# Kernel optimization log

Measured on AMD Instinct MI355X. Metric: run time of the kernel, lower is better.

The kernel has to match this reference:

```python
import jax, jax.numpy as jnp
import numpy as np

C_Z = 128
N_HEADS = 4
HEAD_DIM = 32
TOTAL = N_HEADS * HEAD_DIM
B, N = 1, 256


def setup_inputs() -> dict:
    key = jax.random.key(0)
    ks = jax.random.split(key, 10)
    s = lambda k, sh: jax.random.normal(k, sh, dtype=jnp.float32) * 0.02
    return {
        "pair_representation": jax.random.normal(ks[0], (B, N, N, C_Z), dtype=jnp.float32),
        "ln_gamma": jnp.ones((C_Z,), jnp.float32),
        "ln_beta": jnp.zeros((C_Z,), jnp.float32),
        "Wq": s(ks[1], (C_Z, TOTAL)),
        "Wk": s(ks[2], (C_Z, TOTAL)),
        "Wv": s(ks[3], (C_Z, TOTAL)),
        "Wb": s(ks[4], (C_Z, N_HEADS)),
        "Wg": s(ks[5], (C_Z, TOTAL)),
        "bg": jnp.zeros((TOTAL,), jnp.float32),
        "Wo": s(ks[6], (TOTAL, C_Z)),
        "bo": jnp.zeros((C_Z,), jnp.float32),
    }


def reference(pair_representation, ln_gamma, ln_beta, Wq, Wk, Wv, Wb, Wg, bg, Wo, bo):
    x = pair_representation
    # LayerNorm over c_z
    mu = jnp.mean(x, axis=-1, keepdims=True)
    var = jnp.mean((x - mu) ** 2, axis=-1, keepdims=True)
    x = (x - mu) * jax.lax.rsqrt(var + 1e-5) * ln_gamma + ln_beta

    b, n, _, _ = x.shape
    split = lambda t: t.reshape(b, n, n, N_HEADS, HEAD_DIM)
    Q = split(x @ Wq)  # [b,i,j,h,d]
    K = split(x @ Wk)
    V = split(x @ Wv)
    G = jax.nn.sigmoid(split(x @ Wg + bg))
    Bias = x @ Wb  # [b,j,k,h]

    scores = jnp.einsum("bijhd,bikhd->bijkh", Q, K) / np.float32(np.sqrt(HEAD_DIM))
    scores = scores + Bias[:, None]  # broadcast over i
    attn = jax.nn.softmax(scores, axis=3)  # over k
    vals = jnp.einsum("bijkh,bikhd->bijhd", attn, V)
    vals = (G * vals).reshape(b, n, n, TOTAL)
    return vals @ Wo + bo
```

## Files before the change

kernel.cpp:

```cpp
#include <hip/hip_runtime.h>
#include <hip/hip_bf16.h>


#define QSCALE 0.17677669529663687f

typedef __attribute__((ext_vector_type(8))) short bf16x8;
typedef __attribute__((ext_vector_type(4))) float f32x4;

__device__ __forceinline__ ushort f2bf(float f) {
    uint32_t u = __builtin_bit_cast(uint32_t, f);
    uint32_t r = (u + 0x7FFFu + ((u >> 16) & 1u)) >> 16;
    return (ushort)r;
}
__device__ __forceinline__ float bf2f(ushort b) {
    return __builtin_bit_cast(float, ((uint32_t)b) << 16);
}
__device__ __forceinline__ uint pk2(float a, float b) {
    union { __hip_bfloat162 h; uint u; } cv;
    cv.h = __float22bfloat162_rn(make_float2(a, b));
    return cv.u;
}
__device__ __forceinline__ float4 ld4f(const float* p) { return *(const float4*)p; }

__global__ __launch_bounds__(256) void prep_kernel(
    const float* __restrict__ Wq, const float* __restrict__ Wk, const float* __restrict__ Wv,
    const float* __restrict__ Wb, const float* __restrict__ Wg, const float* __restrict__ Wo,
    ushort* __restrict__ Wfrag, ushort* __restrict__ WoFrag)
{
    int idx = blockIdx.x * 256 + threadIdx.x;
    if (idx < 67584) {
        int j = idx & 7, lane = (idx >> 3) & 63, ks = (idx >> 9) & 3, ct = idx >> 11;
        int n = ct * 16 + (lane & 15);
        int k = ks * 32 + (lane >> 4) * 8 + j;
        float v = 0.f;
        if (n < 128)      v = Wq[k * 128 + n] * QSCALE;
        else if (n < 256) v = Wk[k * 128 + (n - 128)];
        else if (n < 384) v = Wv[k * 128 + (n - 256)];
        else if (n < 512) v = Wg[k * 128 + (n - 384)];
        else if (n < 516) v = Wb[k * 4 + (n - 512)];
        Wfrag[idx] = f2bf(v);
    } else {
        int idx2 = idx - 67584;
        int j = idx2 & 7, lane = (idx2 >> 3) & 63, ks = (idx2 >> 9) & 3, ct = idx2 >> 11;
        int n = ct * 16 + (lane & 15);
        int k = ks * 32 + (lane >> 4) * 8 + j;
        WoFrag[idx2] = f2bf(Wo[k * 128 + n]);
    }
}

__global__ __launch_bounds__(256) void proj_kernel(
    const float* __restrict__ x, const float* __restrict__ gamma, const float* __restrict__ beta,
    const ushort* __restrict__ Wfrag, const float* __restrict__ bg,
    ushort* __restrict__ Qg, ushort* __restrict__ Kg, ushort* __restrict__ Vtg,
    ushort* __restrict__ Gg, float* __restrict__ BbF)
{
    __shared__ ushort Bs[11 * 2048];
    const int t = threadIdx.x;
    const int wave = t >> 6, lane = t & 63, m = lane & 15, quad = lane >> 4;
    const int p0 = blockIdx.x * 64;
    const int arow = p0 + wave * 16 + m;

    float4 xa[4][2];
    float sum = 0.f, ssq = 0.f;
#pragma unroll
    for (int ks = 0; ks < 4; ++ks) {
        const float* rp = x + arow * 128 + ks * 32 + quad * 8;
        xa[ks][0] = ld4f(rp);
        xa[ks][1] = ld4f(rp + 4);
#pragma unroll
        for (int q4 = 0; q4 < 2; ++q4) {
            float4 v = xa[ks][q4];
            sum += v.x + v.y + v.z + v.w;
            ssq += v.x * v.x + v.y * v.y + v.z * v.z + v.w * v.w;
        }
    }
    sum += __shfl_xor(sum, 16); ssq += __shfl_xor(ssq, 16);
    sum += __shfl_xor(sum, 32); ssq += __shfl_xor(ssq, 32);
    const float mu   = sum * (1.f / 128.f);
    const float var  = ssq * (1.f / 128.f) - mu * mu;
    const float rstd = rsqrtf(var + 1e-5f);

    bf16x8 xf[4];
#pragma unroll
    for (int ks = 0; ks < 4; ++ks) {
        union { bf16x8 v; uint u[4]; } xu;
#pragma unroll
        for (int q4 = 0; q4 < 2; ++q4) {
            const int c = ks * 32 + quad * 8 + q4 * 4;
            float4 g4 = ld4f(gamma + c);
            float4 b4 = ld4f(beta + c);
            float4 v = xa[ks][q4];
            float n0 = (v.x - mu) * rstd * g4.x + b4.x;
            float n1 = (v.y - mu) * rstd * g4.y + b4.y;
            float n2 = (v.z - mu) * rstd * g4.z + b4.z;
            float n3 = (v.w - mu) * rstd * g4.w + b4.w;
            xu.u[q4 * 2]     = pk2(n0, n1);
            xu.u[q4 * 2 + 1] = pk2(n2, n3);
        }
        xf[ks] = xu.v;
    }

    const int p = arow;
    const int i = p >> 8, j2 = p & 255;

    for (int phase = 0; phase < 3; ++phase) {
        const int ctbase = phase * 11;
        __syncthreads();
        const uint4* src = (const uint4*)(Wfrag + ctbase * 2048);
        uint4* dst = (uint4*)Bs;
#pragma unroll
        for (int r = 0; r < 11; ++r) dst[r * 256 + t] = src[r * 256 + t];
        __syncthreads();

        for (int ctl = 0; ctl < 11; ++ctl) {
            const int ct = ctbase + ctl;
            f32x4 acc = (f32x4){0.f, 0.f, 0.f, 0.f};
#pragma unroll
            for (int ks = 0; ks < 4; ++ks) {
                bf16x8 wfr = ((const bf16x8*)Bs)[(ctl * 4 + ks) * 64 + lane];
                acc = __builtin_amdgcn_mfma_f32_16x16x32_bf16(wfr, xf[ks], acc, 0, 0, 0);
            }
            if (ct < 32) {
                const int cls = ct >> 3;
                const int npb = (ct & 7) * 16 + quad * 4;
                const int hh = npb >> 5, d0 = npb & 31;
                if (cls == 2) {
                    const int vb = ((i * 4 + hh) * 32 + d0) * 256 + j2;
#pragma unroll
                    for (int r = 0; r < 4; ++r)
                        Vtg[vb + r * 256] = f2bf(acc[r]);
                } else {
                    const int off = ((i * 4 + hh) * 256 + j2) * 32 + d0;
                    uint2 u;
                    if (cls == 3) {
                        float4 bg4 = ld4f(&bg[npb]);
                        float z0 = 1.f / (1.f + __expf(-(acc[0] + bg4.x)));
                        float z1 = 1.f / (1.f + __expf(-(acc[1] + bg4.y)));
                        float z2 = 1.f / (1.f + __expf(-(acc[2] + bg4.z)));
                        float z3 = 1.f / (1.f + __expf(-(acc[3] + bg4.w)));
                        u.x = pk2(z0, z1); u.y = pk2(z2, z3);
                        *(uint2*)(&Gg[off]) = u;
                    } else {
                        u.x = pk2(acc[0], acc[1]); u.y = pk2(acc[2], acc[3]);
                        if (cls == 0) *(uint2*)(&Qg[off]) = u;
                        else          *(uint2*)(&Kg[off]) = u;
                    }
                }
            } else if (quad == 0) {
#pragma unroll
                for (int r = 0; r < 4; ++r) {
                    int addr = (((r * 16 + (i >> 4)) * 16 + (j2 >> 4)) * 64 +
                                ((j2 & 15) >> 2) * 16 + (i & 15)) * 4 + (j2 & 3);
                    BbF[addr] = acc[r];
                }
            }
        }
    }
}

__global__ __launch_bounds__(256) void attn_kernel(
    const ushort* __restrict__ Qg, const ushort* __restrict__ Kg, const ushort* __restrict__ Vtg,
    const ushort* __restrict__ Gg, const float* __restrict__ BbF, ushort* __restrict__ gvals)
{
    __shared__ ushort Pl[4][64 * 72];
    const int t = threadIdx.x;
    const int wave = t >> 6, lane = t & 63, m = lane & 15, quad = lane >> 4;
    const int ih = blockIdx.x, i = ih >> 2, h = ih & 3;

    const int j0 = wave * 64;
    bf16x8 qf[4];
#pragma unroll
    for (int jt = 0; jt < 4; ++jt)
        qf[jt] = *(const bf16x8*)(Qg + ih * 8192 + (j0 + jt * 16 + m) * 32 + quad * 8);

    f32x4 O[4][2];
    float lsum[4];
#pragma unroll
    for (int jt = 0; jt < 4; ++jt) {
        O[jt][0] = (f32x4){0.f, 0.f, 0.f, 0.f};
        O[jt][1] = (f32x4){0.f, 0.f, 0.f, 0.f};
        lsum[jt] = 0.f;
    }

    for (int kt2 = 0; kt2 < 4; ++kt2) {
        const int k0 = kt2 * 64;
        bf16x8 kf[4];
#pragma unroll
        for (int kk = 0; kk < 4; ++kk)
            kf[kk] = *(const bf16x8*)(Kg + ih * 8192 + (k0 + kk * 16 + m) * 32 + quad * 8);

#pragma unroll
        for (int jt = 0; jt < 4; ++jt) {
            const int jtg = wave * 4 + jt;
#pragma unroll
            for (int kk = 0; kk < 4; ++kk) {
                const int ktg = kt2 * 4 + kk;
                f32x4 bias = *(const f32x4*)(BbF + (((h * 16 + jtg) * 16 + ktg) * 64 + lane) * 4);
                f32x4 S = __builtin_amdgcn_mfma_f32_16x16x32_bf16(kf[kk], qf[jt], bias, 0, 0, 0);
                float pv0 = __expf(S[0]);
                float pv1 = __expf(S[1]);
                float pv2 = __expf(S[2]);
                float pv3 = __expf(S[3]);
                lsum[jt] += pv0 + pv1 + pv2 + pv3;
                uint2 u; u.x = pk2(pv0, pv1); u.y = pk2(pv2, pv3);
                *(uint2*)(&Pl[wave][(jt * 16 + m) * 72 + kk * 16 + quad * 4]) = u;
            }
        }
#pragma unroll
        for (int kc = 0; kc < 2; ++kc) {
            bf16x8 pf[4], vf[2];
#pragma unroll
            for (int jt = 0; jt < 4; ++jt)
                pf[jt] = *(const bf16x8*)(&Pl[wave][(jt * 16 + m) * 72 + kc * 32 + quad * 8]);
#pragma unroll
            for (int dt = 0; dt < 2; ++dt)
                vf[dt] = *(const bf16x8*)(Vtg + (ih * 32 + dt * 16 + m) * 256 + k0 + kc * 32 + quad * 8);
#pragma unroll
            for (int jt = 0; jt < 4; ++jt)
#pragma unroll
                for (int dt = 0; dt < 2; ++dt)
                    O[jt][dt] = __builtin_amdgcn_mfma_f32_16x16x32_bf16(
                        vf[dt], pf[jt], O[jt][dt], 0, 0, 0);
        }
    }

#pragma unroll
    for (int jt = 0; jt < 4; ++jt) {
        float s = lsum[jt];
        s += __shfl_xor(s, 16);
        s += __shfl_xor(s, 32);
        lsum[jt] = 1.f / s;
    }

#pragma unroll
    for (int jt = 0; jt < 4; ++jt) {
        const int j = j0 + jt * 16 + m;
        const float rl = lsum[jt];
#pragma unroll
        for (int dt = 0; dt < 2; ++dt) {
            const int d0 = dt * 16 + quad * 4;
            ushort4 gv = *(const ushort4*)(&Gg[ih * 8192 + j * 32 + d0]);
            float v0 = O[jt][dt][0] * rl * bf2f(gv.x);
            float v1 = O[jt][dt][1] * rl * bf2f(gv.y);
            float v2 = O[jt][dt][2] * rl * bf2f(gv.z);
            float v3 = O[jt][dt][3] * rl * bf2f(gv.w);
            uint2 u; u.x = pk2(v0, v1); u.y = pk2(v2, v3);
            *(uint2*)(&gvals[(i * 256 + j) * 128 + h * 32 + d0]) = u;
        }
    }
}

__global__ __launch_bounds__(256) void oproj_kernel(
    const ushort* __restrict__ gvals, const ushort* __restrict__ WoFrag,
    const float* __restrict__ bo, float* __restrict__ out)
{
    __shared__ ushort Bs[8 * 2048];
    const int t = threadIdx.x;
    const int wave = t >> 6, lane = t & 63, m = lane & 15, quad = lane >> 4;
    const int p0 = blockIdx.x * 64;
    {
        const uint4* src = (const uint4*)WoFrag;
        uint4* dst = (uint4*)Bs;
#pragma unroll
        for (int r = 0; r < 8; ++r) dst[r * 256 + t] = src[r * 256 + t];
    }
    bf16x8 gf[4];
    const int p = p0 + wave * 16 + m;
#pragma unroll
    for (int ks = 0; ks < 4; ++ks)
        gf[ks] = *(const bf16x8*)(gvals + p * 128 + ks * 32 + quad * 8);
    __syncthreads();

#pragma unroll
    for (int ct = 0; ct < 8; ++ct) {
        f32x4 acc = (f32x4){0.f, 0.f, 0.f, 0.f};
#pragma unroll
        for (int ks = 0; ks < 4; ++ks) {
            bf16x8 wfr = ((const bf16x8*)Bs)[(ct * 4 + ks) * 64 + lane];
            acc = __builtin_amdgcn_mfma_f32_16x16x32_bf16(wfr, gf[ks], acc, 0, 0, 0);
        }
        const int c0 = ct * 16 + quad * 4;
        float4 bov = ld4f(&bo[c0]);
        float4 v = make_float4(acc[0] + bov.x, acc[1] + bov.y,
                               acc[2] + bov.z, acc[3] + bov.w);
        *(float4*)(&out[p * 128 + c0]) = v;
    }
}

extern "C" void kernel_launch(void* const* d_in, const int* in_sizes, int n_in,
                              void* d_out, int out_size, void* d_ws, size_t ws_size,
                              hipStream_t stream) {
    const float* x     = (const float*)d_in[0];
    const float* gamma = (const float*)d_in[1];
    const float* beta  = (const float*)d_in[2];
    const float* Wq    = (const float*)d_in[3];
    const float* Wk    = (const float*)d_in[4];
    const float* Wv    = (const float*)d_in[5];
    const float* Wb    = (const float*)d_in[6];
    const float* Wg    = (const float*)d_in[7];
    const float* bg    = (const float*)d_in[8];
    const float* Wo    = (const float*)d_in[9];
    const float* bo    = (const float*)d_in[10];

    ushort* ws     = (ushort*)d_ws;
    ushort* Wfrag  = ws;
    ushort* WoFrag = Wfrag + 67584;
    ushort* Qg     = WoFrag + 16384;
    ushort* Kg     = Qg + 8388608;
    ushort* Vtg    = Kg + 8388608;
    ushort* Gg     = Vtg + 8388608;
    ushort* gvals  = Gg + 8388608;
    float*  BbF    = (float*)(gvals + 8388608);

    prep_kernel<<<328, 256, 0, stream>>>(Wq, Wk, Wv, Wb, Wg, Wo, Wfrag, WoFrag);
    proj_kernel<<<1024, 256, 0, stream>>>(x, gamma, beta, Wfrag, bg, Qg, Kg, Vtg, Gg, BbF);
    attn_kernel<<<1024, 256, 0, stream>>>(Qg, Kg, Vtg, Gg, BbF, gvals);
    oproj_kernel<<<1024, 256, 0, stream>>>(gvals, WoFrag, bo, (float*)d_out);
}
```

Before: 171.2 us.

## Fuse projection, attention and output projection into one per-row kernel

Replaces the separate projection, attention and output-projection kernels with a single kernel per row i using 1024 threads. It computes K, V, Q and G for each head on the fly into shared memory and registers, runs softmax attention, then applies the output projection from shared memory. The pair bias moves to a small standalone kernel. This removes the large global round-trips of Q/K/V/G/gvals, in exchange for only 256 blocks, heavy register use, and weights read straight from global memory rather than staged in LDS.

```diff
diff --git a/kernel.cpp b/kernel.cpp
--- a/kernel.cpp
+++ b/kernel.cpp
@@ -12,9 +12,6 @@
     uint32_t r = (u + 0x7FFFu + ((u >> 16) & 1u)) >> 16;
     return (ushort)r;
 }
-__device__ __forceinline__ float bf2f(ushort b) {
-    return __builtin_bit_cast(float, ((uint32_t)b) << 16);
-}
 __device__ __forceinline__ uint pk2(float a, float b) {
     union { __hip_bfloat162 h; uint u; } cv;
     cv.h = __float22bfloat162_rn(make_float2(a, b));
@@ -22,253 +19,262 @@
 }
 __device__ __forceinline__ float4 ld4f(const float* p) { return *(const float4*)p; }
 
+__device__ __forceinline__ bf16x8 xpose(uint2 A, uint2 B, int quad, int m) {
+    int s0 = ((quad & 1) << 5) + m;
+    int s1 = s0 + 16;
+    uint a0 = (uint)__shfl((int)A.x, s0), a1 = (uint)__shfl((int)A.y, s0);
+    uint a2 = (uint)__shfl((int)A.x, s1), a3 = (uint)__shfl((int)A.y, s1);
+    uint b0 = (uint)__shfl((int)B.x, s0), b1 = (uint)__shfl((int)B.y, s0);
+    uint b2 = (uint)__shfl((int)B.x, s1), b3 = (uint)__shfl((int)B.y, s1);
+    bool lo = quad < 2;
+    union { bf16x8 v; uint u[4]; } r;
+    r.u[0] = lo ? a0 : b0;
+    r.u[1] = lo ? a1 : b1;
+    r.u[2] = lo ? a2 : b2;
+    r.u[3] = lo ? a3 : b3;
+    return r.v;
+}
+
 __global__ __launch_bounds__(256) void prep_kernel(
     const float* __restrict__ Wq, const float* __restrict__ Wk, const float* __restrict__ Wv,
-    const float* __restrict__ Wb, const float* __restrict__ Wg, const float* __restrict__ Wo,
+    const float* __restrict__ Wg, const float* __restrict__ Wo,
     ushort* __restrict__ Wfrag, ushort* __restrict__ WoFrag)
 {
     int idx = blockIdx.x * 256 + threadIdx.x;
-    if (idx < 67584) {
-        int j = idx & 7, lane = (idx >> 3) & 63, ks = (idx >> 9) & 3, ct = idx >> 11;
+    if (idx < 65536) {
+        int e = idx & 7, lane = (idx >> 3) & 63, ks = (idx >> 9) & 3, ct = idx >> 11;
         int n = ct * 16 + (lane & 15);
-        int k = ks * 32 + (lane >> 4) * 8 + j;
-        float v = 0.f;
+        int k = ks * 32 + (lane >> 4) * 8 + e;
+        float v;
         if (n < 128)      v = Wq[k * 128 + n] * QSCALE;
         else if (n < 256) v = Wk[k * 128 + (n - 128)];
         else if (n < 384) v = Wv[k * 128 + (n - 256)];
-        else if (n < 512) v = Wg[k * 128 + (n - 384)];
-        else if (n < 516) v = Wb[k * 4 + (n - 512)];
+        else              v = Wg[k * 128 + (n - 384)];
         Wfrag[idx] = f2bf(v);
     } else {
-        int idx2 = idx - 67584;
-        int j = idx2 & 7, lane = (idx2 >> 3) & 63, ks = (idx2 >> 9) & 3, ct = idx2 >> 11;
+        int idx2 = idx - 65536;
+        int e = idx2 & 7, lane = (idx2 >> 3) & 63, ks = (idx2 >> 9) & 3, ct = idx2 >> 11;
         int n = ct * 16 + (lane & 15);
-        int k = ks * 32 + (lane >> 4) * 8 + j;
+        int k = ks * 32 + (lane >> 4) * 8 + e;
         WoFrag[idx2] = f2bf(Wo[k * 128 + n]);
     }
 }
 
-__global__ __launch_bounds__(256) void proj_kernel(
-    const float* __restrict__ x, const float* __restrict__ gamma, const float* __restrict__ beta,
-    const ushort* __restrict__ Wfrag, const float* __restrict__ bg,
-    ushort* __restrict__ Qg, ushort* __restrict__ Kg, ushort* __restrict__ Vtg,
-    ushort* __restrict__ Gg, float* __restrict__ BbF)
+__global__ __launch_bounds__(256) void bias_kernel(
+    const float* __restrict__ x, const float* __restrict__ gamma,
+    const float* __restrict__ beta, const float* __restrict__ Wb,
+    float* __restrict__ BbF)
 {
-    __shared__ ushort Bs[11 * 2048];
     const int t = threadIdx.x;
-    const int wave = t >> 6, lane = t & 63, m = lane & 15, quad = lane >> 4;
-    const int p0 = blockIdx.x * 64;
-    const int arow = p0 + wave * 16 + m;
-
+    const int p = blockIdx.x * 128 + (t >> 1);
+    const int half = t & 1;
+    const float* rp = x + p * 128 + half * 64;
+    float4 v[16];
+    float sum = 0.f, ssq = 0.f;
+#pragma unroll
+    for (int ii = 0; ii < 16; ++ii) {
+        v[ii] = ld4f(rp + ii * 4);
+        sum += v[ii].x + v[ii].y + v[ii].z + v[ii].w;
+        ssq += v[ii].x * v[ii].x + v[ii].y * v[ii].y + v[ii].z * v[ii].z + v[ii].w * v[ii].w;
+    }
+    sum += __shfl_xor(sum, 1);
+    ssq += __shfl_xor(ssq, 1);
+    float mu = sum * (1.f / 128.f);
+    float var = ssq * (1.f / 128.f) - mu * mu;
+    float rstd = rsqrtf(var + 1e-5f);
+
+    float d0 = 0.f, d1 = 0.f, d2 = 0.f, d3 = 0.f;
+#pragma unroll
+    for (int ii = 0; ii < 16; ++ii) {
+        int c = half * 64 + ii * 4;
+        float4 g4 = ld4f(gamma + c), b4 = ld4f(beta + c);
+        float n0 = (v[ii].x - mu) * rstd * g4.x + b4.x;
+        float n1 = (v[ii].y - mu) * rstd * g4.y + b4.y;
+        float n2 = (v[ii].z - mu) * rstd * g4.z + b4.z;
+        float n3 = (v[ii].w - mu) * rstd * g4.w + b4.w;
+        float4 w0 = ld4f(Wb + (c + 0) * 4);
+        float4 w1 = ld4f(Wb + (c + 1) * 4);
+        float4 w2 = ld4f(Wb + (c + 2) * 4);
+        float4 w3 = ld4f(Wb + (c + 3) * 4);
+        d0 += n0 * w0.x + n1 * w1.x + n2 * w2.x + n3 * w3.x;
+        d1 += n0 * w0.y + n1 * w1.y + n2 * w2.y + n3 * w3.y;
+        d2 += n0 * w0.z + n1 * w1.z + n2 * w2.z + n3 * w3.z;
+        d3 += n0 * w0.w + n1 * w1.w + n2 * w2.w + n3 * w3.w;
+    }
+    d0 += __shfl_xor(d0, 1);
+    d1 += __shfl_xor(d1, 1);
+    d2 += __shfl_xor(d2, 1);
+    d3 += __shfl_xor(d3, 1);
+    if (half == 0) {
+        int j = p >> 8, k = p & 255;
+        int base = ((j >> 4) * 16 + (k >> 4)) * 256 + ((k & 15) >> 2) * 64 + (j & 15) * 4 + (k & 3);
+        BbF[base]          = d0;
+        BbF[base + 65536]  = d1;
+        BbF[base + 131072] = d2;
+        BbF[base + 196608] = d3;
+    }
+}
+
+__global__ __launch_bounds__(1024) void fused_kernel(
+    const float* __restrict__ x, const float* __restrict__ gamma,
+    const float* __restrict__ beta, const ushort* __restrict__ Wfrag,
+    const float* __restrict__ bg, const float* __restrict__ BbF,
+    const ushort* __restrict__ WoFrag, const float* __restrict__ bo,
+    float* __restrict__ out)
+{
+    __shared__ ushort smem[32768];
+    ushort* K_s = smem;
+    ushort* V_s = smem + 8192;
+    ushort* GV_s = smem;
+
+    const int t = threadIdx.x;
+    const int w = t >> 6, lane = t & 63, m = lane & 15, quad = lane >> 4;
+    const int i = blockIdx.x;
+
+    const float* xr = x + (i * 256 + w * 16 + m) * 128 + quad * 8;
     float4 xa[4][2];
     float sum = 0.f, ssq = 0.f;
 #pragma unroll
     for (int ks = 0; ks < 4; ++ks) {
-        const float* rp = x + arow * 128 + ks * 32 + quad * 8;
-        xa[ks][0] = ld4f(rp);
-        xa[ks][1] = ld4f(rp + 4);
+        xa[ks][0] = ld4f(xr + ks * 32);
+        xa[ks][1] = ld4f(xr + ks * 32 + 4);
 #pragma unroll
         for (int q4 = 0; q4 < 2; ++q4) {
-            float4 v = xa[ks][q4];
-            sum += v.x + v.y + v.z + v.w;
-            ssq += v.x * v.x + v.y * v.y + v.z * v.z + v.w * v.w;
+            float4 vv = xa[ks][q4];
+            sum += vv.x + vv.y + vv.z + vv.w;
+            ssq += vv.x * vv.x + vv.y * vv.y + vv.z * vv.z + vv.w * vv.w;
         }
     }
     sum += __shfl_xor(sum, 16); ssq += __shfl_xor(ssq, 16);
     sum += __shfl_xor(sum, 32); ssq += __shfl_xor(ssq, 32);
-    const float mu   = sum * (1.f / 128.f);
-    const float var  = ssq * (1.f / 128.f) - mu * mu;
+    const float mu = sum * (1.f / 128.f);
+    const float var = ssq * (1.f / 128.f) - mu * mu;
     const float rstd = rsqrtf(var + 1e-5f);
 
-    bf16x8 xf[4];
+    bf16x8 xnf[4];
 #pragma unroll
     for (int ks = 0; ks < 4; ++ks) {
+        const int c = ks * 32 + quad * 8;
+        float4 g0 = ld4f(gamma + c), g1 = ld4f(gamma + c + 4);
+        float4 b0 = ld4f(beta + c),  b1 = ld4f(beta + c + 4);
+        float4 v0 = xa[ks][0], v1 = xa[ks][1];
         union { bf16x8 v; uint u[4]; } xu;
-#pragma unroll
-        for (int q4 = 0; q4 < 2; ++q4) {
-            const int c = ks * 32 + quad * 8 + q4 * 4;
-            float4 g4 = ld4f(gamma + c);
-            float4 b4 = ld4f(beta + c);
-            float4 v = xa[ks][q4];
-            float n0 = (v.x - mu) * rstd * g4.x + b4.x;
-            float n1 = (v.y - mu) * rstd * g4.y + b4.y;
-            float n2 = (v.z - mu) * rstd * g4.z + b4.z;
-            float n3 = (v.w - mu) * rstd * g4.w + b4.w;
-            xu.u[q4 * 2]     = pk2(n0, n1);
-            xu.u[q4 * 2 + 1] = pk2(n2, n3);
-        }
-        xf[ks] = xu.v;
-    }
-
-    const int p = arow;
-    const int i = p >> 8, j2 = p & 255;
-
-    for (int phase = 0; phase < 3; ++phase) {
-        const int ctbase = phase * 11;
+        xu.u[0] = pk2((v0.x - mu) * rstd * g0.x + b0.x, (v0.y - mu) * rstd * g0.y + b0.y);
+        xu.u[1] = pk2((v0.z - mu) * rstd * g0.z + b0.z, (v0.w - mu) * rstd * g0.w + b0.w);
+        xu.u[2] = pk2((v1.x - mu) * rstd * g1.x + b1.x, (v1.y - mu) * rstd * g1.y + b1.y);
+        xu.u[3] = pk2((v1.z - mu) * rstd * g1.z + b1.z, (v1.w - mu) * rstd * g1.w + b1.w);
+        xnf[ks] = xu.v;
+    }
+
+    uint gst[4][4];
+
+#pragma unroll
+    for (int h = 0; h < 4; ++h) {
+#pragma unroll
+        for (int dt = 0; dt < 2; ++dt) {
+            const int ct = 8 + 2 * h + dt;
+            f32x4 acc = (f32x4){0.f, 0.f, 0.f, 0.f};
+#pragma unroll
+            for (int ks = 0; ks < 4; ++ks) {
+                bf16x8 wf = *(const bf16x8*)(Wfrag + ((ct * 4 + ks) * 64 + lane) * 8);
+                acc = __builtin_amdgcn_mfma_f32_16x16x32_bf16(wf, xnf[ks], acc, 0, 0, 0);
+            }
+            uint2 u; u.x = pk2(acc[0], acc[1]); u.y = pk2(acc[2], acc[3]);
+            *(uint2*)(K_s + (w * 64 + (dt * 2 + (quad >> 1)) * 16 + m) * 8 + (quad & 1) * 4) = u;
+        }
+#pragma unroll
+        for (int dt = 0; dt < 2; ++dt) {
+            const int ct = 16 + 2 * h + dt;
+            f32x4 acc = (f32x4){0.f, 0.f, 0.f, 0.f};
+#pragma unroll
+            for (int ks = 0; ks < 4; ++ks) {
+                bf16x8 wf = *(const bf16x8*)(Wfrag + ((ct * 4 + ks) * 64 + lane) * 8);
+                acc = __builtin_amdgcn_mfma_f32_16x16x32_bf16(xnf[ks], wf, acc, 0, 0, 0);
+            }
+            uint2 u; u.x = pk2(acc[0], acc[1]); u.y = pk2(acc[2], acc[3]);
+            *(uint2*)(V_s + (((w >> 1) * 2 + dt) * 512 +
+                             (((w & 1) * 2 + (quad >> 1)) * 16 + m) * 8 + (quad & 1) * 4)) = u;
+        }
+        uint2 qpk[2];
+#pragma unroll
+        for (int dt = 0; dt < 2; ++dt) {
+            const int ct = 2 * h + dt;
+            f32x4 acc = (f32x4){0.f, 0.f, 0.f, 0.f};
+#pragma unroll
+            for (int ks = 0; ks < 4; ++ks) {
+                bf16x8 wf = *(const bf16x8*)(Wfrag + ((ct * 4 + ks) * 64 + lane) * 8);
+                acc = __builtin_amdgcn_mfma_f32_16x16x32_bf16(wf, xnf[ks], acc, 0, 0, 0);
+            }
+            qpk[dt].x = pk2(acc[0], acc[1]); qpk[dt].y = pk2(acc[2], acc[3]);
+        }
+        bf16x8 qf = xpose(qpk[0], qpk[1], quad, m);
+        f32x4 Gs[2];
+#pragma unroll
+        for (int dt = 0; dt < 2; ++dt) {
+            const int ct = 24 + 2 * h + dt;
+            f32x4 acc = (f32x4){0.f, 0.f, 0.f, 0.f};
+#pragma unroll
+            for (int ks = 0; ks < 4; ++ks) {
+                bf16x8 wf = *(const bf16x8*)(Wfrag + ((ct * 4 + ks) * 64 + lane) * 8);
+                acc = __builtin_amdgcn_mfma_f32_16x16x32_bf16(wf, xnf[ks], acc, 0, 0, 0);
+            }
+            float4 bg4 = ld4f(bg + h * 32 + dt * 16 + quad * 4);
+            Gs[dt][0] = 1.f / (1.f + __expf(-(acc[0] + bg4.x)));
+            Gs[dt][1] = 1.f / (1.f + __expf(-(acc[1] + bg4.y)));
+            Gs[dt][2] = 1.f / (1.f + __expf(-(acc[2] + bg4.z)));
+            Gs[dt][3] = 1.f / (1.f + __expf(-(acc[3] + bg4.w)));
+        }
+
         __syncthreads();
-        const uint4* src = (const uint4*)(Wfrag + ctbase * 2048);
-        uint4* dst = (uint4*)Bs;
-#pragma unroll
-        for (int r = 0; r < 11; ++r) dst[r * 256 + t] = src[r * 256 + t];
+
+        f32x4 O0 = (f32x4){0.f, 0.f, 0.f, 0.f};
+        f32x4 O1 = (f32x4){0.f, 0.f, 0.f, 0.f};
+        float lsum = 0.f;
+        const float* bb = BbF + ((h * 16 + w) * 16) * 256 + lane * 4;
+#pragma unroll
+        for (int kt2 = 0; kt2 < 4; ++kt2) {
+            uint2 spk[4];
+#pragma unroll
+            for (int kk = 0; kk < 4; ++kk) {
+                const int tile = kt2 * 4 + kk;
+                bf16x8 kf = *(const bf16x8*)(K_s + (tile * 64 + lane) * 8);
+                f32x4 bias = *(const f32x4*)(bb + tile * 256);
+                f32x4 S = __builtin_amdgcn_mfma_f32_16x16x32_bf16(kf, qf, bias, 0, 0, 0);
+                float p0 = __expf(S[0]), p1 = __expf(S[1]);
+                float p2 = __expf(S[2]), p3 = __expf(S[3]);
+                lsum += p0 + p1 + p2 + p3;
+                spk[kk].x = pk2(p0, p1); spk[kk].y = pk2(p2, p3);
+            }
+#pragma unroll
+            for (int kc = 0; kc < 2; ++kc) {
+                bf16x8 pf = xpose(spk[kc * 2], spk[kc * 2 + 1], quad, m);
+                const int kcg = kt2 * 2 + kc;
+                bf16x8 vf0 = *(const bf16x8*)(V_s + ((kcg * 2 + 0) * 512 + lane * 8));
+                bf16x8 vf1 = *(const bf16x8*)(V_s + ((kcg * 2 + 1) * 512 + lane * 8));
+                O0 = __builtin_amdgcn_mfma_f32_16x16x32_bf16(vf0, pf, O0, 0, 0, 0);
+                O1 = __builtin_amdgcn_mfma_f32_16x16x32_bf16(vf1, pf, O1, 0, 0, 0);
+            }
+        }
+        lsum += __shfl_xor(lsum, 16);
+        lsum += __shfl_xor(lsum, 32);
+        const float rl = 1.f / lsum;
+        gst[h][0] = pk2(O0[0] * rl * Gs[0][0], O0[1] * rl * Gs[0][1]);
+        gst[h][1] = pk2(O0[2] * rl * Gs[0][2], O0[3] * rl * Gs[0][3]);
+        gst[h][2] = pk2(O1[0] * rl * Gs[1][0], O1[1] * rl * Gs[1][1]);
+        gst[h][3] = pk2(O1[2] * rl * Gs[1][2], O1[3] * rl * Gs[1][3]);
+
         __syncthreads();
-
-        for (int ctl = 0; ctl < 11; ++ctl) {
-            const int ct = ctbase + ctl;
-            f32x4 acc = (f32x4){0.f, 0.f, 0.f, 0.f};
-#pragma unroll
-            for (int ks = 0; ks < 4; ++ks) {
-                bf16x8 wfr = ((const bf16x8*)Bs)[(ctl * 4 + ks) * 64 + lane];
-                acc = __builtin_amdgcn_mfma_f32_16x16x32_bf16(wfr, xf[ks], acc, 0, 0, 0);
-            }
-            if (ct < 32) {
-                const int cls = ct >> 3;
-                const int npb = (ct & 7) * 16 + quad * 4;
-                const int hh = npb >> 5, d0 = npb & 31;
-                if (cls == 2) {
-                    const int vb = ((i * 4 + hh) * 32 + d0) * 256 + j2;
-#pragma unroll
-                    for (int r = 0; r < 4; ++r)
-                        Vtg[vb + r * 256] = f2bf(acc[r]);
-                } else {
-                    const int off = ((i * 4 + hh) * 256 + j2) * 32 + d0;
-                    uint2 u;
-                    if (cls == 3) {
-                        float4 bg4 = ld4f(&bg[npb]);
-                        float z0 = 1.f / (1.f + __expf(-(acc[0] + bg4.x)));
-                        float z1 = 1.f / (1.f + __expf(-(acc[1] + bg4.y)));
-                        float z2 = 1.f / (1.f + __expf(-(acc[2] + bg4.z)));
-                        float z3 = 1.f / (1.f + __expf(-(acc[3] + bg4.w)));
-                        u.x = pk2(z0, z1); u.y = pk2(z2, z3);
-                        *(uint2*)(&Gg[off]) = u;
-                    } else {
-                        u.x = pk2(acc[0], acc[1]); u.y = pk2(acc[2], acc[3]);
-                        if (cls == 0) *(uint2*)(&Qg[off]) = u;
-                        else          *(uint2*)(&Kg[off]) = u;
-                    }
-                }
-            } else if (quad == 0) {
-#pragma unroll
-                for (int r = 0; r < 4; ++r) {
-                    int addr = (((r * 16 + (i >> 4)) * 16 + (j2 >> 4)) * 64 +
-                                ((j2 & 15) >> 2) * 16 + (i & 15)) * 4 + (j2 & 3);
-                    BbF[addr] = acc[r];
-                }
-            }
-        }
-    }
-}
-
-__global__ __launch_bounds__(256) void attn_kernel(
-    const ushort* __restrict__ Qg, const ushort* __restrict__ Kg, const ushort* __restrict__ Vtg,
-    const ushort* __restrict__ Gg, const float* __restrict__ BbF, ushort* __restrict__ gvals)
-{
-    __shared__ ushort Pl[4][64 * 72];
-    const int t = threadIdx.x;
-    const int wave = t >> 6, lane = t & 63, m = lane & 15, quad = lane >> 4;
-    const int ih = blockIdx.x, i = ih >> 2, h = ih & 3;
-
-    const int j0 = wave * 64;
-    bf16x8 qf[4];
-#pragma unroll
-    for (int jt = 0; jt < 4; ++jt)
-        qf[jt] = *(const bf16x8*)(Qg + ih * 8192 + (j0 + jt * 16 + m) * 32 + quad * 8);
-
-    f32x4 O[4][2];
-    float lsum[4];
-#pragma unroll
-    for (int jt = 0; jt < 4; ++jt) {
-        O[jt][0] = (f32x4){0.f, 0.f, 0.f, 0.f};
-        O[jt][1] = (f32x4){0.f, 0.f, 0.f, 0.f};
-        lsum[jt] = 0.f;
-    }
-
-    for (int kt2 = 0; kt2 < 4; ++kt2) {
-        const int k0 = kt2 * 64;
-        bf16x8 kf[4];
-#pragma unroll
-        for (int kk = 0; kk < 4; ++kk)
-            kf[kk] = *(const bf16x8*)(Kg + ih * 8192 + (k0 + kk * 16 + m) * 32 + quad * 8);
-
-#pragma unroll
-        for (int jt = 0; jt < 4; ++jt) {
-            const int jtg = wave * 4 + jt;
-#pragma unroll
-            for (int kk = 0; kk < 4; ++kk) {
-                const int ktg = kt2 * 4 + kk;
-                f32x4 bias = *(const f32x4*)(BbF + (((h * 16 + jtg) * 16 + ktg) * 64 + lane) * 4);
-                f32x4 S = __builtin_amdgcn_mfma_f32_16x16x32_bf16(kf[kk], qf[jt], bias, 0, 0, 0);
-                float pv0 = __expf(S[0]);
-                float pv1 = __expf(S[1]);
-                float pv2 = __expf(S[2]);
-                float pv3 = __expf(S[3]);
-                lsum[jt] += pv0 + pv1 + pv2 + pv3;
-                uint2 u; u.x = pk2(pv0, pv1); u.y = pk2(pv2, pv3);
-                *(uint2*)(&Pl[wave][(jt * 16 + m) * 72 + kk * 16 + quad * 4]) = u;
-            }
-        }
-#pragma unroll
-        for (int kc = 0; kc < 2; ++kc) {
-            bf16x8 pf[4], vf[2];
-#pragma unroll
-            for (int jt = 0; jt < 4; ++jt)
-                pf[jt] = *(const bf16x8*)(&Pl[wave][(jt * 16 + m) * 72 + kc * 32 + quad * 8]);
-#pragma unroll
-            for (int dt = 0; dt < 2; ++dt)
-                vf[dt] = *(const bf16x8*)(Vtg + (ih * 32 + dt * 16 + m) * 256 + k0 + kc * 32 + quad * 8);
-#pragma unroll
-            for (int jt = 0; jt < 4; ++jt)
-#pragma unroll
-                for (int dt = 0; dt < 2; ++dt)
-                    O[jt][dt] = __builtin_amdgcn_mfma_f32_16x16x32_bf16(
-                        vf[dt], pf[jt], O[jt][dt], 0, 0, 0);
-        }
-    }
-
-#pragma unroll
-    for (int jt = 0; jt < 4; ++jt) {
-        float s = lsum[jt];
-        s += __shfl_xor(s, 16);
-        s += __shfl_xor(s, 32);
-        lsum[jt] = 1.f / s;
-    }
-
-#pragma unroll
-    for (int jt = 0; jt < 4; ++jt) {
-        const int j = j0 + jt * 16 + m;
-        const float rl = lsum[jt];
-#pragma unroll
-        for (int dt = 0; dt < 2; ++dt) {
-            const int d0 = dt * 16 + quad * 4;
-            ushort4 gv = *(const ushort4*)(&Gg[ih * 8192 + j * 32 + d0]);
-            float v0 = O[jt][dt][0] * rl * bf2f(gv.x);
-            float v1 = O[jt][dt][1] * rl * bf2f(gv.y);
-            float v2 = O[jt][dt][2] * rl * bf2f(gv.z);
-            float v3 = O[jt][dt][3] * rl * bf2f(gv.w);
-            uint2 u; u.x = pk2(v0, v1); u.y = pk2(v2, v3);
-            *(uint2*)(&gvals[(i * 256 + j) * 128 + h * 32 + d0]) = u;
-        }
-    }
-}
-
-__global__ __launch_bounds__(256) void oproj_kernel(
-    const ushort* __restrict__ gvals, const ushort* __restrict__ WoFrag,
-    const float* __restrict__ bo, float* __restrict__ out)
-{
-    __shared__ ushort Bs[8 * 2048];
-    const int t = threadIdx.x;
-    const int wave = t >> 6, lane = t & 63, m = lane & 15, quad = lane >> 4;
-    const int p0 = blockIdx.x * 64;
-    {
-        const uint4* src = (const uint4*)WoFrag;
-        uint4* dst = (uint4*)Bs;
-#pragma unroll
-        for (int r = 0; r < 8; ++r) dst[r * 256 + t] = src[r * 256 + t];
-    }
-    bf16x8 gf[4];
-    const int p = p0 + wave * 16 + m;
-#pragma unroll
-    for (int ks = 0; ks < 4; ++ks)
-        gf[ks] = *(const bf16x8*)(gvals + p * 128 + ks * 32 + quad * 8);
+    }
+
+#pragma unroll
+    for (int h = 0; h < 4; ++h) {
+#pragma unroll
+        for (int dt = 0; dt < 2; ++dt) {
+            uint2 u; u.x = gst[h][dt * 2]; u.y = gst[h][dt * 2 + 1];
+            *(uint2*)(GV_s + ((w * 4 + h) * 512 +
+                              ((dt * 2 + (quad >> 1)) * 16 + m) * 8 + (quad & 1) * 4)) = u;
+        }
+    }
     __syncthreads();
 
 #pragma unroll
@@ -276,14 +282,14 @@
         f32x4 acc = (f32x4){0.f, 0.f, 0.f, 0.f};
 #pragma unroll
         for (int ks = 0; ks < 4; ++ks) {
-            bf16x8 wfr = ((const bf16x8*)Bs)[(ct * 4 + ks) * 64 + lane];
-            acc = __builtin_amdgcn_mfma_f32_16x16x32_bf16(wfr, gf[ks], acc, 0, 0, 0);
-        }
-        const int c0 = ct * 16 + quad * 4;
-        float4 bov = ld4f(&bo[c0]);
-        float4 v = make_float4(acc[0] + bov.x, acc[1] + bov.y,
-                               acc[2] + bov.z, acc[3] + bov.w);
-        *(float4*)(&out[p * 128 + c0]) = v;
+            bf16x8 wf = *(const bf16x8*)(WoFrag + ((ct * 4 + ks) * 64 + lane) * 8);
+            bf16x8 gf = *(const bf16x8*)(GV_s + ((w * 4 + ks) * 512 + lane * 8));
+            acc = __builtin_amdgcn_mfma_f32_16x16x32_bf16(gf, wf, acc, 0, 0, 0);
+        }
+        const float bov = bo[ct * 16 + m];
+#pragma unroll
+        for (int r = 0; r < 4; ++r)
+            out[(i * 256 + w * 16 + quad * 4 + r) * 128 + ct * 16 + m] = acc[r] + bov;
     }
 }
 
@@ -302,18 +308,12 @@
     const float* Wo    = (const float*)d_in[9];
     const float* bo    = (const float*)d_in[10];
 
-    ushort* ws     = (ushort*)d_ws;
-    ushort* Wfrag  = ws;
-    ushort* WoFrag = Wfrag + 67584;
-    ushort* Qg     = WoFrag + 16384;
-    ushort* Kg     = Qg + 8388608;
-    ushort* Vtg    = Kg + 8388608;
-    ushort* Gg     = Vtg + 8388608;
-    ushort* gvals  = Gg + 8388608;
-    float*  BbF    = (float*)(gvals + 8388608);
-
-    prep_kernel<<<328, 256, 0, stream>>>(Wq, Wk, Wv, Wb, Wg, Wo, Wfrag, WoFrag);
-    proj_kernel<<<1024, 256, 0, stream>>>(x, gamma, beta, Wfrag, bg, Qg, Kg, Vtg, Gg, BbF);
-    attn_kernel<<<1024, 256, 0, stream>>>(Qg, Kg, Vtg, Gg, BbF, gvals);
-    oproj_kernel<<<1024, 256, 0, stream>>>(gvals, WoFrag, bo, (float*)d_out);
-}
+    ushort* Wfrag  = (ushort*)d_ws;
+    ushort* WoFrag = Wfrag + 65536;
+    float*  BbF    = (float*)(WoFrag + 16384);
+
+    prep_kernel<<<320, 256, 0, stream>>>(Wq, Wk, Wv, Wg, Wo, Wfrag, WoFrag);
+    bias_kernel<<<512, 256, 0, stream>>>(x, gamma, beta, Wb, BbF);
+    fused_kernel<<<256, 1024, 0, stream>>>(x, gamma, beta, Wfrag, bg, BbF,
+                                           WoFrag, bo, (float*)d_out);
+}
```

New measurement: 194.4 us. +13.6%, slower.
